# Performance work log

Hardware: AMD Instinct MI355X
Metric: run time of the kernel (lower is better)

## Reference

```python
import jax, jax.numpy as jnp
import numpy as np

B, N, K, C = 8, 4096, 16, 128
HID, DEPTH = 4 * C, 2
EPS = 1e-5


def _bn(x, g, b, m, v):
    # BatchNorm1d in eval mode over the last (channel) dim
    return (x - m) * (g * jax.lax.rsqrt(v + EPS)) + b


def _ffn(x, w1, b1, w2, b2, g, bt, m, v):
    h = jax.nn.relu(jnp.einsum('bnc,ch->bnh', x, w1) + b1)
    y = jnp.einsum('bnh,hc->bnc', h, w2) + b2
    return _bn(y, g, bt, m, v)


def setup_inputs() -> dict:
    key = jax.random.key(0)
    ks = jax.random.split(key, 24)
    s = 0.05
    inp = {
        'x': jax.random.normal(ks[0], (B, N, C), jnp.float32),
        'knn_idx': jax.random.randint(ks[1], (B, N, K), 0, N, jnp.int64),
        'mlp0_w1': jax.random.normal(ks[2], (C, HID), jnp.float32) * s,
        'mlp0_b1': jax.random.normal(ks[3], (HID,), jnp.float32) * s,
        'mlp0_w2': jax.random.normal(ks[4], (HID, C), jnp.float32) * s,
        'mlp0_b2': jax.random.normal(ks[5], (C,), jnp.float32) * s,
        'mlp0_g': jax.random.uniform(ks[6], (C,), jnp.float32, 0.5, 1.5),
        'mlp0_beta': jax.random.normal(ks[7], (C,), jnp.float32) * s,
        'mlp0_m': jnp.zeros((C,), jnp.float32),
        'mlp0_v': jnp.ones((C,), jnp.float32),
        'vfr_w': jax.random.normal(ks[8], (DEPTH, C, C), jnp.float32) * s,
        'vfr_b': jax.random.normal(ks[9], (DEPTH, C), jnp.float32) * s,
        'vfr_g': jax.random.uniform(ks[10], (DEPTH, C), jnp.float32, 0.5, 1.5),
        'vfr_beta': jax.random.normal(ks[11], (DEPTH, C), jnp.float32) * s,
        'vfr_m': jnp.zeros((DEPTH, C), jnp.float32),
        'vfr_v': jnp.ones((DEPTH, C), jnp.float32),
        'ffn_w1': jax.random.normal(ks[12], (DEPTH, C, HID), jnp.float32) * s,
        'ffn_b1': jax.random.normal(ks[13], (DEPTH, HID), jnp.float32) * s,
        'ffn_w2': jax.random.normal(ks[14], (DEPTH, HID, C), jnp.float32) * s,
        'ffn_b2': jax.random.normal(ks[15], (DEPTH, C), jnp.float32) * s,
        'ffn_g': jax.random.uniform(ks[16], (DEPTH, C), jnp.float32, 0.5, 1.5),
        'ffn_beta': jax.random.normal(ks[17], (DEPTH, C), jnp.float32) * s,
        'ffn_m': jnp.zeros((DEPTH, C), jnp.float32),
        'ffn_v': jnp.ones((DEPTH, C), jnp.float32),
    }
    return inp


def reference(x, knn_idx,
              mlp0_w1, mlp0_b1, mlp0_w2, mlp0_b2, mlp0_g, mlp0_beta, mlp0_m, mlp0_v,
              vfr_w, vfr_b, vfr_g, vfr_beta, vfr_m, vfr_v,
              ffn_w1, ffn_b1, ffn_w2, ffn_b2, ffn_g, ffn_beta, ffn_m, ffn_v):
    # eval mode: DropPath is identity, BatchNorm uses running stats
    x = x + _ffn(x, mlp0_w1, mlp0_b1, mlp0_w2, mlp0_b2, mlp0_g, mlp0_beta, mlp0_m, mlp0_v)
    gather = jax.vmap(lambda pts, idx: pts[idx])  # [N,C],[N,K] -> [N,K,C]
    for i in range(DEPTH):
        # VFR: linear -> knn gather -> edge diff -> max over K -> BN
        h = jnp.einsum('bnc,cd->bnd', x, vfr_w[i]) + vfr_b[i]
        nb = gather(h, knn_idx)                      # [B,N,K,C]
        agg = jnp.max(nb - h[:, :, None, :], axis=2)  # [B,N,C]
        x = x + _bn(agg, vfr_g[i], vfr_beta[i], vfr_m[i], vfr_v[i])
        x = x + _ffn(x, ffn_w1[i], ffn_b1[i], ffn_w2[i], ffn_b2[i],
                     ffn_g[i], ffn_beta[i], ffn_m[i], ffn_v[i])
    return x
```

## Files before the change

### kernel.cpp

```cpp
#include <hip/hip_runtime.h>
#include <hip/hip_bf16.h>
#include <stdint.h>

typedef __attribute__((ext_vector_type(8))) __bf16 bf16x8;
typedef __attribute__((ext_vector_type(4))) float floatx4;

#define EPS 1e-5f

__device__ __forceinline__ unsigned short f2bf(float f) {
    union { float f; unsigned int u; } x; x.f = f;
    unsigned int r = x.u + 0x7fffu + ((x.u >> 16) & 1u);
    return (unsigned short)(r >> 16);
}

__device__ __forceinline__ float bf2f(unsigned int u) {
    union { unsigned int u; float f; } x; x.u = u << 16; return x.f;
}

__device__ __forceinline__ void lbar() {
    asm volatile("s_waitcnt lgkmcnt(0)" ::: "memory");
    __builtin_amdgcn_s_barrier();
}

struct Params {
    const float* x_in;
    const int*   knn;
    const float* w1s[3];
    const float* w2s[3];
    const float* vws[2];
    unsigned short* W1P[3];
    unsigned short* W2P[3];
    unsigned short* VTP[2];
    const float* b1s[3];
    const float* b2s[3];
    const float* gs[3];
    const float* bes[3];
    const float* ms[3];
    const float* vvs[3];
    const float* vbb[2];
    const float* vgg[2];
    const float* vbt[2];
    const float* vmm[2];
    const float* vva[2];
    float* xf;
};

__global__ __launch_bounds__(256) void pack2(Params P) {
    const int gtid = blockIdx.x * 256 + threadIdx.x;
    unsigned short v[8];
    if (gtid < 24576) {
        const int t = gtid >> 13;
        const int d = (gtid & 8191) << 3;
        const int hf = d >> 14, w = (d >> 11) & 7, ks = (d >> 9) & 3,
                  q = (d >> 7) & 3, ln = (d >> 3) & 15;
        const float* s1 = P.w1s[t];
        const int hcol = 128 * hf + 16 * w + ln;
        const int kb   = 32 * ks + 8 * q;
#pragma unroll
        for (int j = 0; j < 8; ++j) v[j] = f2bf(s1[(kb + j) * 512 + hcol]);
        uint4 pk;
        pk.x = v[0] | ((unsigned)v[1] << 16); pk.y = v[2] | ((unsigned)v[3] << 16);
        pk.z = v[4] | ((unsigned)v[5] << 16); pk.w = v[6] | ((unsigned)v[7] << 16);
        *(uint4*)&P.W1P[t][d] = pk;
    } else if (gtid < 49152) {
        const int g = gtid - 24576;
        const int t = g >> 13;
        const int d = (g & 8191) << 3;
        const int hf = d >> 14, w = (d >> 11) & 7, ks = (d >> 9) & 3,
                  q = (d >> 7) & 3, ln = (d >> 3) & 15;
        const float* s2 = P.w2s[t];
        const int col = 16 * w + ln;
        const int hb  = 128 * hf + 32 * ks + 8 * q;
#pragma unroll
        for (int j = 0; j < 8; ++j) v[j] = f2bf(s2[(hb + j) * 128 + col]);
        uint4 pk;
        pk.x = v[0] | ((unsigned)v[1] << 16); pk.y = v[2] | ((unsigned)v[3] << 16);
        pk.z = v[4] | ((unsigned)v[5] << 16); pk.w = v[6] | ((unsigned)v[7] << 16);
        *(uint4*)&P.W2P[t][d] = pk;
    } else if (gtid < 53248) {
        const int g = gtid - 49152;
        const int t = g >> 11;
        const int d = (g & 2047) << 3;
        const int w = (d >> 11) & 7, ks = (d >> 9) & 3,
                  q = (d >> 7) & 3, ln = (d >> 3) & 15;
        const float* sv = P.vws[t];
        const int col = 16 * w + ln;
        const int kb  = 32 * ks + 8 * q;
#pragma unroll
        for (int j = 0; j < 8; ++j) v[j] = f2bf(sv[(kb + j) * 128 + col]);
        uint4 pk;
        pk.x = v[0] | ((unsigned)v[1] << 16); pk.y = v[2] | ((unsigned)v[3] << 16);
        pk.z = v[4] | ((unsigned)v[5] << 16); pk.w = v[6] | ((unsigned)v[7] << 16);
        *(uint4*)&P.VTP[t][d] = pk;
    }
}

template <int LOADX, int TE, int TF, int TV>
__global__ __launch_bounds__(512, 4)
void stage(Params P, const float* __restrict__ xold_g,
           const unsigned short* __restrict__ VbIn,
           unsigned short* __restrict__ VbOut)
{
    __shared__ __align__(16) unsigned short xt[8192];
    __shared__ __align__(16) float xf32[8192];
    __shared__ __align__(16) uint2 ht2[2048];
    const int tid  = threadIdx.x;
    const int lane = tid & 63;
    const int w    = tid >> 6;
    const int q    = lane >> 4;
    const int ln   = lane & 15;
    const int sw   = ln & 7;
    const int phys = blockIdx.x;
    const int bid  = (phys & 7) * 64 + (phys >> 3);
    const int p0   = bid << 6;
    const floatx4 zero = {0.f, 0.f, 0.f, 0.f};

    if constexpr (LOADX) {
        const int r = tid >> 3, seg = tid & 7;
        const float4* src = (const float4*)(xold_g + (size_t)(p0 + r) * 128 + seg * 16);
        float4* dstf = (float4*)&xf32[r * 128 + seg * 16];
#pragma unroll
        for (int i = 0; i < 2; ++i) {
            float4 a = src[2 * i];
            float4 b = src[2 * i + 1];
            dstf[2 * i]     = a;
            dstf[2 * i + 1] = b;
            int kq = seg * 2 + i;
            uint4 pk;
            pk.x = (unsigned int)f2bf(a.x) | ((unsigned int)f2bf(a.y) << 16);
            pk.y = (unsigned int)f2bf(a.z) | ((unsigned int)f2bf(a.w) << 16);
            pk.z = (unsigned int)f2bf(b.x) | ((unsigned int)f2bf(b.y) << 16);
            pk.w = (unsigned int)f2bf(b.z) | ((unsigned int)f2bf(b.w) << 16);
            *(uint4*)&xt[(r * 16 + (kq ^ (r & 7))) * 8] = pk;
        }
    }

    if constexpr (TE >= 0) {
        const int c0 = lane << 1;
        float2 gv = *(const float2*)(P.vgg[TE] + c0);
        float2 bv = *(const float2*)(P.vbt[TE] + c0);
        float2 mv = *(const float2*)(P.vmm[TE] + c0);
        float2 vv = *(const float2*)(P.vva[TE] + c0);
        const float sc0 = gv.x * rsqrtf(vv.x + EPS);
        const float sc1 = gv.y * rsqrtf(vv.y + EPS);
#pragma unroll
        for (int it = 0; it < 8; ++it) {
            const int pl = it * 8 + w;
            const int p  = p0 + pl;
            const int b  = p >> 12;
            const size_t rowoff = (size_t)p * 128 + c0;
            unsigned int su = *(const unsigned int*)(VbIn + rowoff);
            const int4* kp4 = (const int4*)(P.knn + (size_t)p * 16);
            int4 ka = kp4[0], kb = kp4[1], kc = kp4[2], kd = kp4[3];
            const unsigned short* vbase = VbIn + (((size_t)b << 12) << 7) + c0;
            float m0 = -3.4e38f, m1 = -3.4e38f;
            unsigned int u;
#define GATH(IDX) u = *(const unsigned int*)(vbase + ((size_t)(IDX) << 7)); \
            m0 = fmaxf(m0, bf2f(u & 0xffffu)); m1 = fmaxf(m1, bf2f(u >> 16));
            GATH(ka.x) GATH(ka.y) GATH(ka.z) GATH(ka.w)
            GATH(kb.x) GATH(kb.y) GATH(kb.z) GATH(kb.w)
            GATH(kc.x) GATH(kc.y) GATH(kc.z) GATH(kc.w)
            GATH(kd.x) GATH(kd.y) GATH(kd.z) GATH(kd.w)
#undef GATH
            float s0 = bf2f(su & 0xffffu), s1 = bf2f(su >> 16);
            float y0 = (m0 - s0 - mv.x) * sc0 + bv.x;
            float y1 = (m1 - s1 - mv.y) * sc1 + bv.y;
            float2 xv = *(const float2*)(xold_g + rowoff);
            float xn0 = xv.x + y0, xn1 = xv.y + y1;
            *(float2*)&xf32[pl * 128 + c0] = make_float2(xn0, xn1);
            unsigned int pk = (unsigned int)f2bf(xn0) | ((unsigned int)f2bf(xn1) << 16);
            ((unsigned int*)xt)[(pl * 16 + ((lane >> 2) ^ (pl & 7))) * 4 + (lane & 3)] = pk;
        }
    }
    lbar();

    floatx4 acc2[4];
#pragma unroll
    for (int i = 0; i < 4; ++i) acc2[i] = zero;

    const unsigned short* W1 = P.W1P[TF];
    const unsigned short* W2 = P.W2P[TF];
    const float* b1 = P.b1s[TF];
    const unsigned short* a1base = W1 + w * 2048 + q * 128 + ln * 8;
    const unsigned short* b2base = W2 + w * 2048 + q * 128 + ln * 8;

    bf16x8 afr[4];
#pragma unroll
    for (int ks = 0; ks < 4; ++ks)
        afr[ks] = *(const bf16x8*)(a1base + ks * 512);

#pragma unroll
    for (int hf = 0; hf < 4; ++hf) {
        bf16x8 bwr[4];
#pragma unroll
        for (int ks = 0; ks < 4; ++ks)
            bwr[ks] = *(const bf16x8*)(b2base + hf * 16384 + ks * 512);

        floatx4 acc1[4];
#pragma unroll
        for (int i = 0; i < 4; ++i) acc1[i] = zero;
#pragma unroll
        for (int ks = 0; ks < 4; ++ks) {
#pragma unroll
            for (int nt = 0; nt < 4; ++nt) {
                bf16x8 bfr = *(const bf16x8*)&xt[((16 * nt + ln) * 16 + ((4 * ks + q) ^ sw)) * 8];
                acc1[nt] = __builtin_amdgcn_mfma_f32_16x16x32_bf16(afr[ks], bfr, acc1[nt], 0, 0, 0);
            }
        }
        {
            const int hid0 = 16 * w + 4 * q;
            const int ghid = 128 * hf + hid0;
            const float bv0 = b1[ghid + 0], bv1 = b1[ghid + 1];
            const float bv2 = b1[ghid + 2], bv3 = b1[ghid + 3];
            const int c16  = hid0 >> 3;
            const int half = q & 1;
#pragma unroll
            for (int nt = 0; nt < 4; ++nt) {
                const int pt = 16 * nt + ln;
                float v0 = acc1[nt][0] + bv0; v0 = v0 > 0.f ? v0 : 0.f;
                float v1 = acc1[nt][1] + bv1; v1 = v1 > 0.f ? v1 : 0.f;
                float v2 = acc1[nt][2] + bv2; v2 = v2 > 0.f ? v2 : 0.f;
                float v3 = acc1[nt][3] + bv3; v3 = v3 > 0.f ? v3 : 0.f;
                uint2 pk;
                pk.x = (unsigned int)f2bf(v0) | ((unsigned int)f2bf(v1) << 16);
                pk.y = (unsigned int)f2bf(v2) | ((unsigned int)f2bf(v3) << 16);
                ht2[(pt * 16 + (c16 ^ (pt & 7))) * 2 + half] = pk;
            }
        }
        lbar();
        if (hf < 3) {
#pragma unroll
            for (int ks = 0; ks < 4; ++ks)
                afr[ks] = *(const bf16x8*)(a1base + (hf + 1) * 16384 + ks * 512);
        }
#pragma unroll
        for (int ks = 0; ks < 4; ++ks) {
#pragma unroll
            for (int mt = 0; mt < 4; ++mt) {
                bf16x8 ah = *(const bf16x8*)&ht2[((16 * mt + ln) * 16 + ((4 * ks + q) ^ sw)) * 2];
                acc2[mt] = __builtin_amdgcn_mfma_f32_16x16x32_bf16(ah, bwr[ks], acc2[mt], 0, 0, 0);
            }
        }
        lbar();
    }

    bf16x8 vwr[4];
    if constexpr (TV >= 0) {
        const unsigned short* bb2 = P.VTP[TV] + w * 2048 + q * 128 + ln * 8;
#pragma unroll
        for (int ks = 0; ks < 4; ++ks)
            vwr[ks] = *(const bf16x8*)(bb2 + ks * 512);
    }

    {
        const float* b2   = P.b2s[TF];
        const float* gam  = P.gs[TF];
        const float* bet  = P.bes[TF];
        const float* mean = P.ms[TF];
        const float* var  = P.vvs[TF];
        const int c = 16 * w + ln;
        const float bia = b2[c];
        const float sc  = gam[c] * rsqrtf(var[c] + EPS);
        const float bb  = bet[c];
        const float mu  = mean[c];
#pragma unroll
        for (int mt = 0; mt < 4; ++mt) {
#pragma unroll
            for (int r = 0; r < 4; ++r) {
                const int rl = 16 * mt + 4 * q + r;
                float v  = acc2[mt][r] + bia;
                float y  = (v - mu) * sc + bb;
                float xn = xf32[rl * 128 + c] + y;
                P.xf[(size_t)(p0 + rl) * 128 + c] = xn;
                if constexpr (TV >= 0)
                    xt[(rl * 16 + ((c >> 3) ^ (rl & 7))) * 8 + (c & 7)] = f2bf(xn);
            }
        }
    }

    if constexpr (TV >= 0) {
        lbar();
        const float* vb = P.vbb[TV];
        floatx4 acc[4];
#pragma unroll
        for (int i = 0; i < 4; ++i) acc[i] = zero;
#pragma unroll
        for (int ks = 0; ks < 4; ++ks) {
#pragma unroll
            for (int mt = 0; mt < 4; ++mt) {
                bf16x8 ax = *(const bf16x8*)&xt[((16 * mt + ln) * 16 + ((4 * ks + q) ^ sw)) * 8];
                acc[mt] = __builtin_amdgcn_mfma_f32_16x16x32_bf16(ax, vwr[ks], acc[mt], 0, 0, 0);
            }
        }
        const int c = 16 * w + ln;
        const float bia = vb[c];
#pragma unroll
        for (int mt = 0; mt < 4; ++mt)
#pragma unroll
            for (int r = 0; r < 4; ++r)
                VbOut[(size_t)(p0 + 16 * mt + 4 * q + r) * 128 + c] = f2bf(acc[mt][r] + bia);
    }
}

extern "C" void kernel_launch(void* const* d_in, const int* in_sizes, int n_in,
                              void* d_out, int out_size, void* d_ws, size_t ws_size,
                              hipStream_t stream)
{
    Params p;
    p.x_in = (const float*)d_in[0];
    p.knn  = (const int*)d_in[1];
    const float* w1  = (const float*)d_in[2];
    const float* b1  = (const float*)d_in[3];
    const float* w2  = (const float*)d_in[4];
    const float* b2  = (const float*)d_in[5];
    const float* g0  = (const float*)d_in[6];
    const float* be0 = (const float*)d_in[7];
    const float* m0p = (const float*)d_in[8];
    const float* v0p = (const float*)d_in[9];
    const float* vw  = (const float*)d_in[10];
    const float* vbp = (const float*)d_in[11];
    const float* vgp = (const float*)d_in[12];
    const float* vbe = (const float*)d_in[13];
    const float* vmp = (const float*)d_in[14];
    const float* vvp = (const float*)d_in[15];
    const float* fw1 = (const float*)d_in[16];
    const float* fb1 = (const float*)d_in[17];
    const float* fw2 = (const float*)d_in[18];
    const float* fb2 = (const float*)d_in[19];
    const float* fg  = (const float*)d_in[20];
    const float* fbe = (const float*)d_in[21];
    const float* fm  = (const float*)d_in[22];
    const float* fv  = (const float*)d_in[23];

    p.w1s[0] = w1;  p.w1s[1] = fw1; p.w1s[2] = fw1 + 65536;
    p.w2s[0] = w2;  p.w2s[1] = fw2; p.w2s[2] = fw2 + 65536;
    p.vws[0] = vw;  p.vws[1] = vw + 16384;
    p.b1s[0] = b1;  p.b1s[1] = fb1; p.b1s[2] = fb1 + 512;
    p.b2s[0] = b2;  p.b2s[1] = fb2; p.b2s[2] = fb2 + 128;
    p.gs[0]  = g0;  p.gs[1]  = fg;  p.gs[2]  = fg + 128;
    p.bes[0] = be0; p.bes[1] = fbe; p.bes[2] = fbe + 128;
    p.ms[0]  = m0p; p.ms[1]  = fm;  p.ms[2]  = fm + 128;
    p.vvs[0] = v0p; p.vvs[1] = fv;  p.vvs[2] = fv + 128;
    p.vbb[0] = vbp; p.vbb[1] = vbp + 128;
    p.vgg[0] = vgp; p.vgg[1] = vgp + 128;
    p.vbt[0] = vbe; p.vbt[1] = vbe + 128;
    p.vmm[0] = vmp; p.vmm[1] = vmp + 128;
    p.vva[0] = vvp; p.vva[1] = vvp + 128;

    char* ws = (char*)d_ws;
    unsigned short* Vb0 = (unsigned short*)ws;
    unsigned short* Vb1 = (unsigned short*)(ws + (size_t)(8 << 20));
    unsigned short* u   = (unsigned short*)(ws + (size_t)(16 << 20));
    for (int i = 0; i < 3; ++i) p.W1P[i] = u + i * 65536;
    for (int i = 0; i < 3; ++i) p.W2P[i] = u + 196608 + i * 65536;
    for (int i = 0; i < 2; ++i) p.VTP[i] = u + 393216 + i * 16384;
    p.xf = (float*)d_out;

    pack2<<<dim3(208), 256, 0, stream>>>(p);
    stage<1, -1, 0, 0><<<dim3(512), 512, 0, stream>>>(p, p.x_in, nullptr, Vb0);
    stage<0,  0, 1, 1><<<dim3(512), 512, 0, stream>>>(p, p.xf, Vb0, Vb1);
    stage<0,  1, 2, -1><<<dim3(512), 512, 0, stream>>>(p, p.xf, Vb1, nullptr);
}
```

Baseline: 183.9 us.

## Software-pipeline FFN GEMM1 and GEMM2 across hidden chunks with double-buffered LDS

Double-buffers the hidden-activation LDS tile so that the first GEMM for hidden chunk hf is interleaved with the second GEMM for chunk hf-1, and weight prefetches are issued earlier. This drops one barrier per chunk and gives the scheduler independent MFMA chains to overlap with LDS reads. In exchange it uses an extra 16KB of LDS, which may reduce occupancy under the 4-blocks-per-CU launch bound, and raises register pressure.

```diff
diff --git a/kernel.cpp b/kernel.cpp
--- a/kernel.cpp
+++ b/kernel.cpp
@@ -103,7 +103,7 @@
 {
     __shared__ __align__(16) unsigned short xt[8192];
     __shared__ __align__(16) float xf32[8192];
-    __shared__ __align__(16) uint2 ht2[2048];
+    __shared__ __align__(16) uint2 ht2[2][2048];
     const int tid  = threadIdx.x;
     const int lane = tid & 63;
     const int w    = tid >> 6;
@@ -185,17 +185,35 @@
     const unsigned short* b2base = W2 + w * 2048 + q * 128 + ln * 8;
 
     bf16x8 afr[4];
-#pragma unroll
-    for (int ks = 0; ks < 4; ++ks)
+    bf16x8 bwr[4];
+#pragma unroll
+    for (int ks = 0; ks < 4; ++ks) {
         afr[ks] = *(const bf16x8*)(a1base + ks * 512);
-
-#pragma unroll
-    for (int hf = 0; hf < 4; ++hf) {
-        bf16x8 bwr[4];
-#pragma unroll
-        for (int ks = 0; ks < 4; ++ks)
-            bwr[ks] = *(const bf16x8*)(b2base + hf * 16384 + ks * 512);
-
+        bwr[ks] = *(const bf16x8*)(b2base + ks * 512);
+    }
+
+    auto e1 = [&](int hf, int buf, floatx4* acc1) {
+        const int hid0 = 16 * w + 4 * q;
+        const int ghid = 128 * hf + hid0;
+        const float bv0 = b1[ghid + 0], bv1 = b1[ghid + 1];
+        const float bv2 = b1[ghid + 2], bv3 = b1[ghid + 3];
+        const int c16  = hid0 >> 3;
+        const int half = q & 1;
+#pragma unroll
+        for (int nt = 0; nt < 4; ++nt) {
+            const int pt = 16 * nt + ln;
+            float v0 = acc1[nt][0] + bv0; v0 = v0 > 0.f ? v0 : 0.f;
+            float v1 = acc1[nt][1] + bv1; v1 = v1 > 0.f ? v1 : 0.f;
+            float v2 = acc1[nt][2] + bv2; v2 = v2 > 0.f ? v2 : 0.f;
+            float v3 = acc1[nt][3] + bv3; v3 = v3 > 0.f ? v3 : 0.f;
+            uint2 pk;
+            pk.x = (unsigned int)f2bf(v0) | ((unsigned int)f2bf(v1) << 16);
+            pk.y = (unsigned int)f2bf(v2) | ((unsigned int)f2bf(v3) << 16);
+            ht2[buf][(pt * 16 + (c16 ^ (pt & 7))) * 2 + half] = pk;
+        }
+    };
+
+    {
         floatx4 acc1[4];
 #pragma unroll
         for (int i = 0; i < 4; ++i) acc1[i] = zero;
@@ -207,41 +225,46 @@
                 acc1[nt] = __builtin_amdgcn_mfma_f32_16x16x32_bf16(afr[ks], bfr, acc1[nt], 0, 0, 0);
             }
         }
-        {
-            const int hid0 = 16 * w + 4 * q;
-            const int ghid = 128 * hf + hid0;
-            const float bv0 = b1[ghid + 0], bv1 = b1[ghid + 1];
-            const float bv2 = b1[ghid + 2], bv3 = b1[ghid + 3];
-            const int c16  = hid0 >> 3;
-            const int half = q & 1;
+#pragma unroll
+        for (int ks = 0; ks < 4; ++ks)
+            afr[ks] = *(const bf16x8*)(a1base + 16384 + ks * 512);
+        e1(0, 0, acc1);
+    }
+    lbar();
+
+#pragma unroll
+    for (int hf = 1; hf < 4; ++hf) {
+        const int rbuf = (hf - 1) & 1;
+        floatx4 acc1[4];
+#pragma unroll
+        for (int i = 0; i < 4; ++i) acc1[i] = zero;
+#pragma unroll
+        for (int ks = 0; ks < 4; ++ks) {
 #pragma unroll
             for (int nt = 0; nt < 4; ++nt) {
-                const int pt = 16 * nt + ln;
-                float v0 = acc1[nt][0] + bv0; v0 = v0 > 0.f ? v0 : 0.f;
-                float v1 = acc1[nt][1] + bv1; v1 = v1 > 0.f ? v1 : 0.f;
-                float v2 = acc1[nt][2] + bv2; v2 = v2 > 0.f ? v2 : 0.f;
-                float v3 = acc1[nt][3] + bv3; v3 = v3 > 0.f ? v3 : 0.f;
-                uint2 pk;
-                pk.x = (unsigned int)f2bf(v0) | ((unsigned int)f2bf(v1) << 16);
-                pk.y = (unsigned int)f2bf(v2) | ((unsigned int)f2bf(v3) << 16);
-                ht2[(pt * 16 + (c16 ^ (pt & 7))) * 2 + half] = pk;
+                bf16x8 bfr = *(const bf16x8*)&xt[((16 * nt + ln) * 16 + ((4 * ks + q) ^ sw)) * 8];
+                acc1[nt] = __builtin_amdgcn_mfma_f32_16x16x32_bf16(afr[ks], bfr, acc1[nt], 0, 0, 0);
+                bf16x8 ah = *(const bf16x8*)&ht2[rbuf][((16 * nt + ln) * 16 + ((4 * ks + q) ^ sw)) * 2];
+                acc2[nt] = __builtin_amdgcn_mfma_f32_16x16x32_bf16(ah, bwr[ks], acc2[nt], 0, 0, 0);
             }
         }
+#pragma unroll
+        for (int ks = 0; ks < 4; ++ks) {
+            bwr[ks] = *(const bf16x8*)(b2base + hf * 16384 + ks * 512);
+            if (hf < 3)
+                afr[ks] = *(const bf16x8*)(a1base + (hf + 1) * 16384 + ks * 512);
+        }
+        e1(hf, hf & 1, acc1);
         lbar();
-        if (hf < 3) {
-#pragma unroll
-            for (int ks = 0; ks < 4; ++ks)
-                afr[ks] = *(const bf16x8*)(a1base + (hf + 1) * 16384 + ks * 512);
-        }
-#pragma unroll
-        for (int ks = 0; ks < 4; ++ks) {
-#pragma unroll
-            for (int mt = 0; mt < 4; ++mt) {
-                bf16x8 ah = *(const bf16x8*)&ht2[((16 * mt + ln) * 16 + ((4 * ks + q) ^ sw)) * 2];
-                acc2[mt] = __builtin_amdgcn_mfma_f32_16x16x32_bf16(ah, bwr[ks], acc2[mt], 0, 0, 0);
-            }
-        }
-        lbar();
+    }
+
+#pragma unroll
+    for (int ks = 0; ks < 4; ++ks) {
+#pragma unroll
+        for (int mt = 0; mt < 4; ++mt) {
+            bf16x8 ah = *(const bf16x8*)&ht2[1][((16 * mt + ln) * 16 + ((4 * ks + q) ^ sw)) * 2];
+            acc2[mt] = __builtin_amdgcn_mfma_f32_16x16x32_bf16(ah, bwr[ks], acc2[mt], 0, 0, 0);
+        }
     }
 
     bf16x8 vwr[4];
```

Result: no change. 183.1 us (-0.4%).
